# Kernel optimization log

Measured on AMD Instinct MI355X. Metric: run time of the kernel, lower is better.

## Reference

```python
import jax, jax.numpy as jnp
import numpy as np

L, B, IN, H, OUT = 4, 4096, 1024, 1024, 1024


def setup_inputs() -> dict:
    key = jax.random.key(0)
    ks = jax.random.split(key, 9)
    std = 1.0 / (H + IN) ** 0.5
    return {
        "x": jax.random.normal(ks[0], (B, IN), jnp.float32),
        "h_prev": jax.random.normal(ks[1], (L, B, H), jnp.float32),
        "c_prev": jax.random.normal(ks[2], (L, B, H), jnp.float32),
        "Wi": jax.random.uniform(ks[3], (L, IN, 4 * H), jnp.float32, -std, std),
        "Wh": jax.random.uniform(ks[4], (L, H, 4 * H), jnp.float32, -std, std),
        "bi": jax.random.uniform(ks[5], (L, 4 * H), jnp.float32, -std, std),
        "bh": jax.random.uniform(ks[6], (L, 4 * H), jnp.float32, -std, std),
        "fc_W": jax.random.uniform(ks[7], (H, OUT), jnp.float32, -std, std),
        "fc_b": jax.random.uniform(ks[8], (OUT,), jnp.float32, -std, std),
    }


def _lstm_cell(x, h, c, Wi, Wh, bi, bh):
    # gates: [B, 4H], split into (input, forget, cell, output)
    gates = x @ Wi + bi + h @ Wh + bh
    i, f, g, o = jnp.split(gates, 4, axis=1)
    i, f, o = jax.nn.sigmoid(i), jax.nn.sigmoid(f), jax.nn.sigmoid(o)
    g = jnp.tanh(g)
    c_cur = f * c + i * g
    h_cur = o * jnp.tanh(c_cur)
    return h_cur, c_cur


def reference(x, h_prev, c_prev, Wi, Wh, bi, bh, fc_W, fc_b):
    h_out, c_out = [], []
    x_in = x
    for l in range(L):  # fixed small layer loop
        h_cur, c_cur = _lstm_cell(x_in, h_prev[l], c_prev[l], Wi[l], Wh[l], bi[l], bh[l])
        h_out.append(h_cur)
        c_out.append(c_cur)
        x_in = h_cur
    h_out = jnp.stack(h_out, axis=0)
    c_out = jnp.stack(c_out, axis=0)
    y = h_out[-1] @ fc_W + fc_b
    return y, h_out, c_out
```

## Files before the change

### kernel.cpp

```cpp
#include <hip/hip_runtime.h>

#define B_    4096
#define H_    1024
#define NLAY  4

typedef __attribute__((ext_vector_type(8))) short bf16x8;
typedef __attribute__((ext_vector_type(4))) short s16x4;
typedef __attribute__((ext_vector_type(4))) float f32x4;
typedef unsigned short ushort_t;

__device__ __forceinline__ ushort_t f2bf(float f) {
  unsigned u = __builtin_bit_cast(unsigned, f);
  u += 0x7FFFu + ((u >> 16) & 1u);
  return (ushort_t)(u >> 16);
}

__device__ __forceinline__ float fast_sigmoid(float x) {
  float e = __expf(-fabsf(x));
  float s = 1.0f / (1.0f + e);
  return x >= 0.0f ? s : 1.0f - s;
}
__device__ __forceinline__ float fast_tanh(float x) {
  float e = __expf(-2.0f * fabsf(x));
  float t = (1.0f - e) / (1.0f + e);
  return x >= 0.0f ? t : -t;
}

#define GLDS16(gsrc, ldst)                                                  \
  __builtin_amdgcn_global_load_lds(                                         \
      (__attribute__((address_space(1))) void*)(gsrc),                      \
      (__attribute__((address_space(3))) void*)(ldst), 16, 0, 0)

#define BAR()                                                               \
  { asm volatile("" ::: "memory");                                          \
    __builtin_amdgcn_s_barrier();                                           \
    asm volatile("" ::: "memory"); }

#define WAITV(N)                                                            \
  { asm volatile("s_waitcnt vmcnt(" #N ")" ::: "memory");                   \
    __builtin_amdgcn_sched_barrier(0); }

#define LGKM0()                                                             \
  { asm volatile("s_waitcnt lgkmcnt(0)" ::: "memory");                      \
    __builtin_amdgcn_sched_barrier(0); }

__device__ __forceinline__ bf16x8 dsr128(unsigned addr, int imm) {
  bf16x8 r;
  asm volatile("ds_read_b128 %0, %1 offset:%c2"
               : "=v"(r)
               : "v"(addr), "i"(imm));
  return r;
}

__global__ __launch_bounds__(512, 2) void lstm8(
    const ushort_t* __restrict__ aX, const ushort_t* __restrict__ aH,
    const float* __restrict__ cprev, const float* __restrict__ bi,
    const float* __restrict__ bh, const ushort_t* __restrict__ wtl,
    float* __restrict__ hout, float* __restrict__ cout,
    ushort_t* __restrict__ hbfout) {
  __shared__ __align__(16) char sL[131072];

  const int tid  = threadIdx.x;
  const int lane = tid & 63;
  const int wid  = tid >> 6;
  const int wm   = wid >> 2;
  const int wn   = wid & 3;
  const int bid  = (blockIdx.x & 7) * 32 + (blockIdx.x >> 3);
  const int bm   = bid & 15;
  const int bn   = bid >> 4;

  const int fr = lane & 15;
  const int oF = lane >> 4;
  const int sw = (oF ^ ((fr >> 1) & 3)) * 16;

  const unsigned sBase = (unsigned)(size_t)&sL[0];
  const unsigned aAddr = sBase + (unsigned)(wm * 16384 + fr * 64 + sw);
  const unsigned bAddr = sBase + (unsigned)(65536 + (wn >> 1) * 16384 +
                                            (wn & 1) * 4096 + fr * 64 + sw);

  const int oA = (tid & 3) ^ ((tid >> 3) & 3);
  const size_t aOff0 = (size_t)(bm * 256 + (tid >> 2)) * 1024 + oA * 8;
  const size_t aOff1 = aOff0 + (size_t)128 * 1024;
  const ushort_t* wtBn = wtl + (size_t)bn * 524288;

  f32x4 acc[8][4];
#pragma unroll
  for (int m = 0; m < 8; ++m)
#pragma unroll
    for (int g = 0; g < 4; ++g) acc[m][g] = (f32x4){0.f, 0.f, 0.f, 0.f};

  bf16x8 ar[4][2], br0[2][2], br1[2][2];

#define STAGE_A(PAR, HALF, TT)                                               \
  {                                                                          \
    const ushort_t* s0 =                                                     \
        (((TT) < 16) ? aX : aH) + ((HALF) ? aOff1 : aOff0) + ((TT) & 15) * 64; \
    char* d = sL + (PAR) * 32768 + (HALF) * 16384 + wid * 1024;              \
    GLDS16(s0, d);                                                           \
    GLDS16(s0 + 32, d + 8192);                                               \
  }
#define STAGE_B(PAR, HALF, TT)                                               \
  {                                                                          \
    const ushort_t* s0 =                                                     \
        wtBn + (size_t)((TT) & 31) * 16384 + (HALF) * 8192 + tid * 8;        \
    char* d = sL + 65536 + (PAR) * 32768 + (HALF) * 16384 + wid * 1024;      \
    GLDS16(s0, d);                                                           \
    GLDS16(s0 + 4096, d + 8192);                                             \
  }
#define RD_A(PAR, MH)                                                        \
  _Pragma("unroll") for (int mp = 0; mp < 4; ++mp)                           \
      _Pragma("unroll") for (int kh = 0; kh < 2; ++kh)                       \
      ar[mp][kh] = dsr128(aAddr, (PAR) * 32768 + kh * 8192 +                 \
                                     ((MH) * 4 + mp) * 1024);
#define RD_B(PAR, NH, BR)                                                    \
  _Pragma("unroll") for (int gg = 0; gg < 2; ++gg)                           \
      _Pragma("unroll") for (int kh = 0; kh < 2; ++kh)                       \
      BR[gg][kh] = dsr128(bAddr, (PAR) * 32768 + kh * 8192 +                 \
                                     ((NH) * 2 + gg) * 1024);
#define MM(MH, NH, BR)                                                       \
  __builtin_amdgcn_s_setprio(1);                                             \
  _Pragma("unroll") for (int gg = 0; gg < 2; ++gg)                           \
      _Pragma("unroll") for (int mp = 0; mp < 4; ++mp)                       \
      _Pragma("unroll") for (int kh = 0; kh < 2; ++kh)                       \
      acc[(MH) * 4 + mp][(NH) * 2 + gg] =                                    \
          __builtin_amdgcn_mfma_f32_16x16x32_bf16(                           \
              ar[mp][kh], BR[gg][kh], acc[(MH) * 4 + mp][(NH) * 2 + gg],     \
              0, 0, 0);                                                      \
  __builtin_amdgcn_s_setprio(0);

  STAGE_A(0, 0, 0)
  STAGE_A(0, 1, 0)
  STAGE_B(0, 0, 0)
  STAGE_B(0, 1, 0)
  STAGE_B(1, 0, 1)
  STAGE_B(1, 1, 1)
  WAITV(4)
  BAR()

#pragma unroll 1
  for (int t2 = 0; t2 < 30; t2 += 2) {
    RD_A(0, 0) RD_B(0, 0, br0)
    STAGE_A(1, 0, t2 + 1)
    BAR()
    LGKM0()
    MM(0, 0, br0)
    BAR()

    RD_B(0, 1, br1)
    STAGE_A(1, 1, t2 + 1)
    BAR()
    LGKM0()
    MM(0, 1, br1)
    BAR()

    RD_A(0, 1)
    STAGE_B(0, 0, (t2 + 2))
    BAR()
    LGKM0()
    MM(1, 0, br0)
    BAR()

    STAGE_B(0, 1, (t2 + 2))
    BAR()
    MM(1, 1, br1)
    WAITV(4)
    BAR()

    RD_A(1, 0) RD_B(1, 0, br0)
    STAGE_A(0, 0, (t2 + 2))
    BAR()
    LGKM0()
    MM(0, 0, br0)
    BAR()

    RD_B(1, 1, br1)
    STAGE_A(0, 1, (t2 + 2))
    BAR()
    LGKM0()
    MM(0, 1, br1)
    BAR()

    RD_A(1, 1)
    STAGE_B(1, 0, (t2 + 3))
    BAR()
    LGKM0()
    MM(1, 0, br0)
    BAR()

    STAGE_B(1, 1, (t2 + 3))
    BAR()
    MM(1, 1, br1)
    WAITV(4)
    BAR()
  }

  float cpv[8][4];
  {
    RD_A(0, 0) RD_B(0, 0, br0)
    STAGE_A(1, 0, 31)
    BAR()
    LGKM0()
    MM(0, 0, br0)
    BAR()

    RD_B(0, 1, br1)
    STAGE_A(1, 1, 31)
    BAR()
    LGKM0()
    MM(0, 1, br1)
    BAR()

    RD_A(0, 1)
    {
      const float* cpT = cprev +
                         (size_t)(bm * 256 + wm * 128 + oF * 4) * 1024 +
                         bn * 64 + wn * 16 + fr;
#pragma unroll
      for (int m = 0; m < 8; ++m)
#pragma unroll
        for (int r = 0; r < 4; ++r)
          cpv[m][r] = cpT[(size_t)(m * 16 + r) * 1024];
    }
    BAR()
    LGKM0()
    MM(1, 0, br0)
    BAR()

    BAR()
    MM(1, 1, br1)
    WAITV(32)
    BAR()

    RD_A(1, 0) RD_B(1, 0, br0)
    BAR()
    LGKM0()
    MM(0, 0, br0)
    BAR()

    RD_B(1, 1, br1)
    BAR()
    LGKM0()
    MM(0, 1, br1)
    BAR()

    RD_A(1, 1)
    BAR()
    LGKM0()
    MM(1, 0, br0)
    BAR()

    BAR()
    MM(1, 1, br1)
    WAITV(0)
  }
#undef STAGE_A
#undef STAGE_B
#undef RD_A
#undef RD_B
#undef MM

  __syncthreads();

  const int hcolL = wn * 16 + fr;
  const int hcol  = bn * 64 + hcolL;
  float bsum[4];
#pragma unroll
  for (int g = 0; g < 4; ++g)
    bsum[g] = bi[g * 1024 + hcol] + bh[g * 1024 + hcol];

  float cv[8][4], hv[8][4];
#pragma unroll
  for (int m = 0; m < 8; ++m) {
#pragma unroll
    for (int r = 0; r < 4; ++r) {
      const float gi = fast_sigmoid(acc[m][0][r] + bsum[0]);
      const float gf = fast_sigmoid(acc[m][1][r] + bsum[1]);
      const float gg = fast_tanh(acc[m][2][r] + bsum[2]);
      const float go = fast_sigmoid(acc[m][3][r] + bsum[3]);
      const float c  = gf * cpv[m][r] + gi * gg;
      cv[m][r] = c;
      hv[m][r] = go * fast_tanh(c);
    }
  }

#define LSTRIDE 68
  float* LF = (float*)sL;
  const int crow = tid >> 4;
  const int cc4  = (tid & 15) * 4;
#pragma unroll
  for (int m = 0; m < 8; ++m) {
    const int rowb = wm * 128 + m * 16 + oF * 4;
#pragma unroll
    for (int r = 0; r < 4; ++r) LF[(rowb + r) * LSTRIDE + hcolL] = cv[m][r];
  }
  __syncthreads();
  {
    float* co0 = cout + (size_t)(bm * 256) * 1024 + bn * 64;
#pragma unroll
    for (int i = 0; i < 8; ++i) {
      const int row = i * 32 + crow;
      f32x4 v = *(const f32x4*)(LF + row * LSTRIDE + cc4);
      *(f32x4*)(co0 + (size_t)row * 1024 + cc4) = v;
    }
  }
  __syncthreads();
#pragma unroll
  for (int m = 0; m < 8; ++m) {
    const int rowb = wm * 128 + m * 16 + oF * 4;
#pragma unroll
    for (int r = 0; r < 4; ++r) LF[(rowb + r) * LSTRIDE + hcolL] = hv[m][r];
  }
  __syncthreads();
  {
    float* ho0 = hout + (size_t)(bm * 256) * 1024 + bn * 64;
    ushort_t* hb0 = hbfout + (size_t)(bm * 256) * 1024 + bn * 64;
#pragma unroll
    for (int i = 0; i < 8; ++i) {
      const int row = i * 32 + crow;
      f32x4 v = *(const f32x4*)(LF + row * LSTRIDE + cc4);
      *(f32x4*)(ho0 + (size_t)row * 1024 + cc4) = v;
      s16x4 hb;
#pragma unroll
      for (int j = 0; j < 4; ++j) hb[j] = (short)f2bf(v[j]);
      *(s16x4*)(hb0 + (size_t)row * 1024 + cc4) = hb;
    }
  }
#undef LSTRIDE
}

__global__ __launch_bounds__(512) void packW(const float* __restrict__ Wi,
                                             const float* __restrict__ Wh,
                                             ushort_t* __restrict__ wt) {
  __shared__ ushort_t t16[64 * 257];
  const int bn = blockIdx.x;
  const int T  = blockIdx.y;
  const int l  = blockIdx.z;
  const int tid = threadIdx.x;
  const int kq = tid >> 6, cc = tid & 63;
  const int k0 = T * 64;
  const float* W = (k0 < 1024)
                       ? (Wi + (size_t)l * 1024 * 4096 + (size_t)k0 * 4096)
                       : (Wh + (size_t)l * 1024 * 4096 + (size_t)(k0 - 1024) * 4096);
#pragma unroll
  for (int kk = 0; kk < 8; ++kk) {
    const int kl = kq * 8 + kk;
#pragma unroll
    for (int g = 0; g < 4; ++g) {
      const float v = W[(size_t)kl * 4096 + g * 1024 + bn * 64 + cc];
      const int p = (cc >> 4) * 64 + g * 16 + (cc & 15);
      t16[kl * 257 + p] = f2bf(v);
    }
  }
  __syncthreads();
#pragma unroll
  for (int half = 0; half < 2; ++half) {
    ushort_t* img =
        wt + (((size_t)l * 16 + bn) * 32 + T) * 16384 + half * 8192;
#pragma unroll
    for (int c = 0; c < 2; ++c) {
      const int idx = c * 512 + tid;
      const int kh = idx >> 9;
      const int r  = (idx >> 2) & 127;
      const int s  = idx & 3;
      const int o  = s ^ ((r >> 1) & 3);
      const int klb = kh * 32 + o * 8;
      const int pg  = half * 128 + r;
      bf16x8 ov;
#pragma unroll
      for (int j = 0; j < 8; ++j) ov[j] = (short)t16[(klb + j) * 257 + pg];
      *(bf16x8*)(img + (size_t)idx * 8) = ov;
    }
  }
}

__device__ __forceinline__ int swz(int row, int kelem) {
  return ((row * 64 + kelem) * 2) ^ ((row & 7) << 4);
}

__global__ __launch_bounds__(512) void fc_kernel(
    const ushort_t* __restrict__ wtfc, const ushort_t* __restrict__ abf,
    const float* __restrict__ bias, float* __restrict__ y) {
  __shared__ __align__(16) char sA[128 * 64 * 2];
  __shared__ __align__(16) char sB[64 * 64 * 2];
  const int tid  = threadIdx.x;
  const int lane = tid & 63;
  const int wid  = tid >> 6;
  const int wm   = wid >> 2;
  const int wn   = wid & 3;
  const int bid  = (blockIdx.x & 7) * 64 + (blockIdx.x >> 3);
  const int bm   = bid & 31;
  const int bn   = bid >> 5;

  f32x4 acc[4];
#pragma unroll
  for (int m = 0; m < 4; ++m) acc[m] = (f32x4){0.f, 0.f, 0.f, 0.f};

  const int rloc = wid * 8 + (lane >> 3);
  const int jA   = (lane & 7) ^ ((lane >> 3) & 7);
  const ushort_t* aSrc = abf + (size_t)(bm * 128 + rloc) * 1024 + jA * 8;

  for (int ks = 0; ks < 16; ++ks) {
    __syncthreads();
    GLDS16(wtfc + (size_t)(bn * 16 + ks) * 4096 + tid * 8, sB + wid * 1024);
    const int off = ks * 64;
    GLDS16(aSrc + off,             sA + wid * 1024);
    GLDS16(aSrc + off + 64 * 1024, sA + 8192 + wid * 1024);
    __syncthreads();
#pragma unroll
    for (int kk = 0; kk < 64; kk += 32) {
      const int ke = kk + (lane >> 4) * 8;
      bf16x8 a[4];
#pragma unroll
      for (int m = 0; m < 4; ++m)
        a[m] = *(const bf16x8*)(sA + swz(wm * 64 + m * 16 + (lane & 15), ke));
      bf16x8 b = *(const bf16x8*)(sB + swz(wn * 16 + (lane & 15), ke));
#pragma unroll
      for (int m = 0; m < 4; ++m)
        acc[m] = __builtin_amdgcn_mfma_f32_16x16x32_bf16(a[m], b, acc[m], 0, 0, 0);
    }
  }
  const int col = bn * 64 + wn * 16 + (lane & 15);
  const float bb = bias[col];
#pragma unroll
  for (int m = 0; m < 4; ++m) {
    const int row0 = bm * 128 + wm * 64 + m * 16 + ((lane >> 4) << 2);
#pragma unroll
    for (int r = 0; r < 4; ++r)
      y[(size_t)(row0 + r) * 1024 + col] = acc[m][r] + bb;
  }
}

__global__ __launch_bounds__(512) void transposeFc(const float* __restrict__ W,
                                                   ushort_t* __restrict__ wt) {
  const int bn = blockIdx.x;
  const int ks = blockIdx.y;
  const int tid = threadIdx.x;
  const int c  = tid & 63;
  const int ko = (tid >> 6) * 8;
  float v[8];
#pragma unroll
  for (int j = 0; j < 8; ++j)
    v[j] = W[(size_t)(ks * 64 + ko + j) * 1024 + bn * 64 + c];
  bf16x8 o;
#pragma unroll
  for (int j = 0; j < 8; ++j) o[j] = (short)f2bf(v[j]);
  ushort_t* tile = wt + ((size_t)bn * 16 + ks) * 4096;
  *(bf16x8*)((char*)tile + swz(c, ko)) = o;
}

__global__ __launch_bounds__(256) void cvt_bf16_2(const float* __restrict__ s0,
                                                  unsigned n0,
                                                  const float* __restrict__ s1,
                                                  ushort_t* __restrict__ d0,
                                                  ushort_t* __restrict__ d1,
                                                  unsigned ntot) {
  const unsigned i = blockIdx.x * 256 + threadIdx.x;
  if (i >= ntot) return;
  const float* p;
  ushort_t* d;
  unsigned j;
  if (i < n0) {
    p = s0; d = d0; j = i;
  } else {
    p = s1; d = d1; j = i - n0;
  }
  const float* pp = p + (size_t)j * 8;
  f32x4 a = ((const f32x4*)pp)[0];
  f32x4 b = ((const f32x4*)pp)[1];
  bf16x8 o;
#pragma unroll
  for (int k = 0; k < 4; ++k) {
    o[k]     = (short)f2bf(a[k]);
    o[4 + k] = (short)f2bf(b[k]);
  }
  *(bf16x8*)(d + (size_t)j * 8) = o;
}

extern "C" void kernel_launch(void* const* d_in, const int* in_sizes, int n_in,
                              void* d_out, int out_size, void* d_ws,
                              size_t ws_size, hipStream_t stream) {
  const float* x     = (const float*)d_in[0];
  const float* hprev = (const float*)d_in[1];
  const float* cprev = (const float*)d_in[2];
  const float* Wi    = (const float*)d_in[3];
  const float* Wh    = (const float*)d_in[4];
  const float* bi    = (const float*)d_in[5];
  const float* bh    = (const float*)d_in[6];
  const float* fcW   = (const float*)d_in[7];
  const float* fcb   = (const float*)d_in[8];

  float* out = (float*)d_out;
  const size_t BH = (size_t)B_ * H_;
  float* y    = out;
  float* hout = out + BH;
  float* cout = out + 5 * BH;

  const size_t WT_ELEMS = (size_t)4 * 16 * 32 * 16384;
  const size_t FC_ELEMS = (size_t)16 * 16 * 4096;
  ushort_t* wt      = (ushort_t*)d_ws;
  ushort_t* fcwt    = wt + WT_ELEMS;
  ushort_t* xbf     = fcwt + FC_ELEMS;
  ushort_t* hprevbf = xbf + BH;
  ushort_t* houtbf  = hprevbf + 4 * BH;

  packW<<<dim3(16, 32, 4), dim3(512), 0, stream>>>(Wi, Wh, wt);
  transposeFc<<<dim3(16, 16), dim3(512), 0, stream>>>(fcW, fcwt);
  {
    const unsigned n0 = (unsigned)(BH / 8);
    const unsigned n1 = (unsigned)(4 * BH / 8);
    const unsigned nt = n0 + n1;
    cvt_bf16_2<<<dim3((nt + 255) / 256), dim3(256), 0, stream>>>(
        x, n0, hprev, xbf, hprevbf, nt);
  }

  for (int l = 0; l < NLAY; ++l) {
    const ushort_t* aX  = (l == 0) ? xbf : (houtbf + (size_t)(l - 1) * BH);
    const ushort_t* wtl = wt + (size_t)l * 16 * 32 * 16384;
    lstm8<<<dim3(256), dim3(512), 0, stream>>>(
        aX, hprevbf + (size_t)l * BH, cprev + (size_t)l * BH, bi + l * 4096,
        bh + l * 4096, wtl, hout + (size_t)l * BH, cout + (size_t)l * BH,
        houtbf + (size_t)l * BH);
  }
  fc_kernel<<<dim3(512), dim3(512), 0, stream>>>(fcwt, houtbf + 3 * BH, fcb, y);
}
```

Before: 408.3 us.

## Stage c_prev tile into LDS with async global-to-LDS loads during the K tail

Replaces the per-thread strided scalar loads of c_prev into registers with coalesced 16-byte global-to-LDS copies, issued in four quarter pieces interleaved with the last MFMA iterations. The epilogue then reads c_prev from LDS, writes the new c in place, and stores it out from the same LDS layout, which drops the 32-register cpv array and the separate c staging pass. The change relies on LDS regions being free of A/B data at each staging point and on correct vmcnt waits. An aliasing or ordering mistake would silently corrupt operands, and the unpadded 256-byte row stride may cause bank conflicts in the epilogue.

```diff
diff --git a/kernel.cpp b/kernel.cpp
--- a/kernel.cpp
+++ b/kernel.cpp
@@ -106,6 +106,16 @@
     char* d = sL + 65536 + (PAR) * 32768 + (HALF) * 16384 + wid * 1024;      \
     GLDS16(s0, d);                                                           \
     GLDS16(s0 + 4096, d + 8192);                                             \
+  }
+#define STAGE_CP(Q, QB)                                                      \
+  {                                                                          \
+    _Pragma("unroll") for (int c = 0; c < 2; ++c) {                          \
+      const int j = c * 512 + tid;                                           \
+      const float* s0 = cprev +                                              \
+                        (size_t)(bm * 256 + (Q) * 64 + (j >> 4)) * 1024 +    \
+                        bn * 64 + (j & 15) * 4;                              \
+      GLDS16(s0, sL + (QB) + c * 8192 + wid * 1024);                         \
+    }                                                                        \
   }
 #define RD_A(PAR, MH)                                                        \
   _Pragma("unroll") for (int mp = 0; mp < 4; ++mp)                           \
@@ -194,7 +204,6 @@
     BAR()
   }
 
-  float cpv[8][4];
   {
     RD_A(0, 0) RD_B(0, 0, br0)
     STAGE_A(1, 0, 31)
@@ -211,33 +220,27 @@
     BAR()
 
     RD_A(0, 1)
-    {
-      const float* cpT = cprev +
-                         (size_t)(bm * 256 + wm * 128 + oF * 4) * 1024 +
-                         bn * 64 + wn * 16 + fr;
-#pragma unroll
-      for (int m = 0; m < 8; ++m)
-#pragma unroll
-        for (int r = 0; r < 4; ++r)
-          cpv[m][r] = cpT[(size_t)(m * 16 + r) * 1024];
-    }
+    STAGE_CP(0, 65536)
     BAR()
     LGKM0()
     MM(1, 0, br0)
     BAR()
 
+    STAGE_CP(1, 81920)
     BAR()
     MM(1, 1, br1)
-    WAITV(32)
+    WAITV(4)
     BAR()
 
     RD_A(1, 0) RD_B(1, 0, br0)
+    STAGE_CP(2, 0)
     BAR()
     LGKM0()
     MM(0, 0, br0)
     BAR()
 
     RD_B(1, 1, br1)
+    STAGE_CP(3, 16384)
     BAR()
     LGKM0()
     MM(0, 1, br1)
@@ -255,6 +258,7 @@
   }
 #undef STAGE_A
 #undef STAGE_B
+#undef STAGE_CP
 #undef RD_A
 #undef RD_B
 #undef MM
@@ -268,64 +272,66 @@
   for (int g = 0; g < 4; ++g)
     bsum[g] = bi[g * 1024 + hcol] + bh[g * 1024 + hcol];
 
-  float cv[8][4], hv[8][4];
+  float hv[8][4];
 #pragma unroll
   for (int m = 0; m < 8; ++m) {
+    const int qbase = (wm ? 0 : 65536) + (m >> 2) * 16384;
+    const int rloc  = (m & 3) * 16 + oF * 4;
 #pragma unroll
     for (int r = 0; r < 4; ++r) {
+      float* cpp = (float*)(sL + qbase + (rloc + r) * 256 + hcolL * 4);
+      const float cp = *cpp;
       const float gi = fast_sigmoid(acc[m][0][r] + bsum[0]);
       const float gf = fast_sigmoid(acc[m][1][r] + bsum[1]);
       const float gg = fast_tanh(acc[m][2][r] + bsum[2]);
       const float go = fast_sigmoid(acc[m][3][r] + bsum[3]);
-      const float c  = gf * cpv[m][r] + gi * gg;
-      cv[m][r] = c;
+      const float c  = gf * cp + gi * gg;
+      *cpp = c;
       hv[m][r] = go * fast_tanh(c);
     }
-  }
-
-#define LSTRIDE 68
-  float* LF = (float*)sL;
-  const int crow = tid >> 4;
-  const int cc4  = (tid & 15) * 4;
-#pragma unroll
-  for (int m = 0; m < 8; ++m) {
-    const int rowb = wm * 128 + m * 16 + oF * 4;
-#pragma unroll
-    for (int r = 0; r < 4; ++r) LF[(rowb + r) * LSTRIDE + hcolL] = cv[m][r];
   }
   __syncthreads();
   {
     float* co0 = cout + (size_t)(bm * 256) * 1024 + bn * 64;
+    const int crow = tid >> 4;
+    const int cb   = (tid & 15) * 16;
 #pragma unroll
     for (int i = 0; i < 8; ++i) {
       const int row = i * 32 + crow;
-      f32x4 v = *(const f32x4*)(LF + row * LSTRIDE + cc4);
-      *(f32x4*)(co0 + (size_t)row * 1024 + cc4) = v;
+      const int ab  = ((row < 128) ? 65536 : 0) + ((row >> 6) & 1) * 16384 +
+                      (row & 63) * 256 + cb;
+      f32x4 v = *(const f32x4*)(sL + ab);
+      *(f32x4*)(co0 + (size_t)row * 1024 + (tid & 15) * 4) = v;
     }
   }
   __syncthreads();
 #pragma unroll
   for (int m = 0; m < 8; ++m) {
-    const int rowb = wm * 128 + m * 16 + oF * 4;
-#pragma unroll
-    for (int r = 0; r < 4; ++r) LF[(rowb + r) * LSTRIDE + hcolL] = hv[m][r];
+    const int qbase = (wm ? 0 : 65536) + (m >> 2) * 16384;
+    const int rloc  = (m & 3) * 16 + oF * 4;
+#pragma unroll
+    for (int r = 0; r < 4; ++r)
+      *(float*)(sL + qbase + (rloc + r) * 256 + hcolL * 4) = hv[m][r];
   }
   __syncthreads();
   {
     float* ho0 = hout + (size_t)(bm * 256) * 1024 + bn * 64;
     ushort_t* hb0 = hbfout + (size_t)(bm * 256) * 1024 + bn * 64;
+    const int crow = tid >> 4;
+    const int cb   = (tid & 15) * 16;
 #pragma unroll
     for (int i = 0; i < 8; ++i) {
       const int row = i * 32 + crow;
-      f32x4 v = *(const f32x4*)(LF + row * LSTRIDE + cc4);
-      *(f32x4*)(ho0 + (size_t)row * 1024 + cc4) = v;
+      const int ab  = ((row < 128) ? 65536 : 0) + ((row >> 6) & 1) * 16384 +
+                      (row & 63) * 256 + cb;
+      f32x4 v = *(const f32x4*)(sL + ab);
+      *(f32x4*)(ho0 + (size_t)row * 1024 + (tid & 15) * 4) = v;
       s16x4 hb;
 #pragma unroll
       for (int j = 0; j < 4; ++j) hb[j] = (short)f2bf(v[j]);
-      *(s16x4*)(hb0 + (size_t)row * 1024 + cc4) = hb;
+      *(s16x4*)(hb0 + (size_t)row * 1024 + (tid & 15) * 4) = hb;
     }
   }
-#undef LSTRIDE
 }
 
 __global__ __launch_bounds__(512) void packW(const float* __restrict__ Wi,
```

Result: faster. 372.0 us (-8.9%).
